# Optimization experiments

Hardware: AMD Instinct MI355X
Metric: run time of the kernel (lower is better)

The kernel has to match this reference:

```python
import jax, jax.numpy as jnp
import numpy as np

B, H, W, C = 1, 64, 64, 256
HEADS, K, DIL = 8, 7, 2
HD = C // HEADS
FF = 4 * C
EPS = 1e-5
SCALE = 1.0 / float(np.sqrt(HD))


def _axis_indices(L, k, d):
    """NATTEN dilated neighborhood: per dilation-group clamped sliding window.
    Returns key indices [L,k] and relative-position-bias indices [L,k]."""
    i = np.arange(L)
    g, rem = i // d, i % d                      # position within dilation group
    lg = (L - rem + d - 1) // d                 # group length per position
    start = np.clip(g - k // 2, 0, lg - k)      # clamped window start (group coords)
    a = np.arange(k)
    kidx = (start[:, None] + a[None, :]) * d + rem[:, None]          # key coord
    bidx = start[:, None] + a[None, :] - g[:, None] + (k - 1)        # rpb coord in [0, 2k-2]
    return kidx.astype(np.int32), bidx.astype(np.int32)


def setup_inputs():
    key = jax.random.key(0)
    ks = jax.random.split(key, 8)
    p = lambda k_, sh: jax.random.normal(k_, sh, jnp.float32) * 0.02
    return {
        "x": jax.random.normal(ks[0], (B, H, W, C), jnp.float32),
        "ln1_g": jnp.ones((C,), jnp.float32), "ln1_b": jnp.zeros((C,), jnp.float32),
        "wq": p(ks[1], (C, C)), "bq": jnp.zeros((C,), jnp.float32),
        "wk": p(ks[2], (C, C)), "bk": jnp.zeros((C,), jnp.float32),
        "wv": p(ks[3], (C, C)), "bv": jnp.zeros((C,), jnp.float32),
        "rpb": p(ks[4], (HEADS, 2 * K - 1, 2 * K - 1)),
        "wo": p(ks[5], (C, C)), "bo": jnp.zeros((C,), jnp.float32),
        "ln2_g": jnp.ones((C,), jnp.float32), "ln2_b": jnp.zeros((C,), jnp.float32),
        "w1": p(ks[6], (C, FF)), "b1": jnp.zeros((FF,), jnp.float32),
        "w2": p(ks[7], (FF, C)), "b2": jnp.zeros((C,), jnp.float32),
    }


def _layer_norm(x, g, b):
    m = jnp.mean(x, -1, keepdims=True)
    v = jnp.mean(jnp.square(x - m), -1, keepdims=True)
    return (x - m) * jax.lax.rsqrt(v + EPS) * g + b


def reference(x, ln1_g, ln1_b, wq, bq, wk, bk, wv, bv, rpb, wo, bo,
              ln2_g, ln2_b, w1, b1, w2, b2):
    ih, bih = _axis_indices(H, K, DIL)   # [H,K]
    iw, biw = _axis_indices(W, K, DIL)   # [W,K]
    hs = _layer_norm(x, ln1_g, ln1_b)
    q = (hs @ wq + bq).reshape(B, H, W, HEADS, HD) * SCALE
    k = (hs @ wk + bk).reshape(B, H, W, HEADS, HD)
    v = (hs @ wv + bv).reshape(B, H, W, HEADS, HD)
    # gather dilated neighborhoods -> [B,H,W,K,K,heads,hd]
    k_nb = k[:, ih[:, None, :, None], iw[None, :, None, :], :, :]
    v_nb = v[:, ih[:, None, :, None], iw[None, :, None, :], :, :]
    # natten2dqkrpb: per-query scores over K*K dilated neighbors + rpb
    scores = jnp.einsum('bijnc,bijklnc->bnijkl', q, k_nb)
    bias = rpb[:, bih[:, None, :, None], biw[None, :, None, :]]  # [heads,H,W,K,K]
    scores = scores + bias[None]
    probs = jax.nn.softmax(scores.reshape(B, HEADS, H, W, K * K), axis=-1)
    # natten2dav
    ctx = jnp.einsum('bnijp,bijpnc->bijnc', probs,
                     v_nb.reshape(B, H, W, K * K, HEADS, HD))
    attn_out = ctx.reshape(B, H, W, C) @ wo + bo
    hs2 = x + attn_out                      # residual (layer_scale disabled: init 0.0)
    y = _layer_norm(hs2, ln2_g, ln2_b)
    y = jax.nn.gelu(y @ w1 + b1, approximate=False) @ w2 + b2
    return hs2 + y
```

## Files before the change

### kernel.cpp

```cpp
#include <hip/hip_runtime.h>
#include <math.h>

#define CC 256
#define NTOK 4096
#define NHEADS 8
#define HD 32
#define FFD 1024
#define LN_EPS 1e-5f
#define QSCALE 0.17677669529663687f

typedef __bf16 bf16x8 __attribute__((ext_vector_type(8)));
typedef float f32x4 __attribute__((ext_vector_type(4)));
typedef unsigned short u16x8 __attribute__((ext_vector_type(8)));

__device__ __forceinline__ unsigned short f2bf(float f) {
    unsigned u = __builtin_bit_cast(unsigned, f);
    u += 0x7fff + ((u >> 16) & 1);
    return (unsigned short)(u >> 16);
}
__device__ __forceinline__ float bf2f(unsigned short h) {
    unsigned u = ((unsigned)h) << 16;
    return __builtin_bit_cast(float, u);
}
__device__ __forceinline__ void gload16(const unsigned short* g, unsigned short* l) {
    __builtin_amdgcn_global_load_lds(
        (const __attribute__((address_space(1))) unsigned int*)(const void*)g,
        (__attribute__((address_space(3))) unsigned int*)(void*)l, 16, 0, 0);
}

__global__ void ln_kernel(const float* __restrict__ x, const float* __restrict__ g,
                          const float* __restrict__ b, unsigned short* __restrict__ out) {
    int wave = threadIdx.x >> 6;
    int lane = threadIdx.x & 63;
    int tok = blockIdx.x * 4 + wave;
    const float4 v = ((const float4*)(x + (size_t)tok * CC))[lane];
    float s  = v.x + v.y + v.z + v.w;
    float ss = v.x * v.x + v.y * v.y + v.z * v.z + v.w * v.w;
    #pragma unroll
    for (int o = 32; o > 0; o >>= 1) { s += __shfl_xor(s, o); ss += __shfl_xor(ss, o); }
    float m   = s * (1.0f / CC);
    float var = ss * (1.0f / CC) - m * m;
    float r   = rsqrtf(var + LN_EPS);
    float4 gv = ((const float4*)g)[lane];
    float4 bv = ((const float4*)b)[lane];
    ushort4 o4;
    o4.x = f2bf((v.x - m) * r * gv.x + bv.x);
    o4.y = f2bf((v.y - m) * r * gv.y + bv.y);
    o4.z = f2bf((v.z - m) * r * gv.z + bv.z);
    o4.w = f2bf((v.w - m) * r * gv.w + bv.w);
    ((ushort4*)(out + (size_t)tok * CC))[lane] = o4;
}

__global__ void setup_kernel(const float* __restrict__ wq, const float* __restrict__ wk,
                             const float* __restrict__ wv, const float* __restrict__ wo,
                             const float* __restrict__ w1, const float* __restrict__ w2,
                             const float* __restrict__ bq, const float* __restrict__ bk,
                             const float* __restrict__ bv,
                             unsigned short* __restrict__ wt_qkv, unsigned short* __restrict__ wo_t,
                             unsigned short* __restrict__ w1_t, unsigned short* __restrict__ w2_t,
                             float* __restrict__ bqkv) {
    int id = blockIdx.x;
    int t = threadIdx.x;
    if (id == 192) {
        bqkv[t]       = bq[t] * QSCALE;
        bqkv[256 + t] = bk[t];
        bqkv[512 + t] = bv[t];
        return;
    }
    const float* src; unsigned short* dst;
    int Kd, N, rowoff = 0, bx, by; float scale = 1.0f;
    if (id < 16)       { src = wq; dst = wt_qkv; Kd = 256;  N = 256;  scale = QSCALE; int l = id;       bx = l & 3;  by = l >> 2; }
    else if (id < 32)  { src = wk; dst = wt_qkv; Kd = 256;  N = 256;  rowoff = 256;   int l = id - 16;  bx = l & 3;  by = l >> 2; }
    else if (id < 48)  { src = wv; dst = wt_qkv; Kd = 256;  N = 256;  rowoff = 512;   int l = id - 32;  bx = l & 3;  by = l >> 2; }
    else if (id < 64)  { src = wo; dst = wo_t;   Kd = 256;  N = 256;                  int l = id - 48;  bx = l & 3;  by = l >> 2; }
    else if (id < 128) { src = w1; dst = w1_t;   Kd = 256;  N = 1024;                 int l = id - 64;  bx = l & 15; by = l >> 4; }
    else               { src = w2; dst = w2_t;   Kd = 1024; N = 256;                  int l = id - 128; bx = l & 3;  by = l >> 2; }
    int n0 = bx * 64, k0 = by * 64;
    __shared__ float tile[64][65];
    int cc = t & 63, rb = t >> 6;
    #pragma unroll
    for (int i = 0; i < 16; i++) {
        int r = rb + i * 4;
        tile[r][cc] = src[(size_t)(k0 + r) * N + n0 + cc];
    }
    __syncthreads();
    int n = t >> 2;
    #pragma unroll
    for (int i = 0; i < 8; i++) {
        int p = (t & 3) + i * 4;
        unsigned lo = f2bf(tile[2 * p][n] * scale);
        unsigned hi = f2bf(tile[2 * p + 1][n] * scale);
        *(unsigned*)(dst + (size_t)(rowoff + n0 + n) * Kd + k0 + 2 * p) = lo | (hi << 16);
    }
}

template<int BM, int BN, int KD, int ACT, bool ADD_RES, bool OUT_BF16>
__global__ __launch_bounds__(256) void gemm_db(
    const unsigned short* __restrict__ A, const unsigned short* __restrict__ Bt,
    const float* __restrict__ bias, const float* __restrict__ res,
    void* __restrict__ Cm, int N) {
    constexpr int WM = BM / 2, WN = BN / 2;
    constexpr int MF = WM / 16, NF = WN / 16;
    constexpr int NIT = KD / 64;
    __shared__ unsigned short lds[2][(BM + BN) * 64];
    const int t = threadIdx.x;
    const int lane = t & 63, w = t >> 6;
    const int wr = w >> 1, wc = w & 1;
    const int bm = blockIdx.y * BM, bn = blockIdx.x * BN;
    const int fr = lane & 15, sq = lane >> 4;

    auto stage = [&](int it, int buf) {
        unsigned short* La = lds[buf];
        unsigned short* Lb = lds[buf] + BM * 64;
        #pragma unroll
        for (int i = 0; i < BM * 8 / 256; i++) {
            int c = t + i * 256;
            int kk = c / (BM * 4), r = (c % (BM * 4)) >> 2, jj = c & 3;
            gload16(A + (size_t)(bm + r) * KD + it * 64 + kk * 32 + jj * 8, La + c * 8);
        }
        #pragma unroll
        for (int i = 0; i < BN * 8 / 256; i++) {
            int c = t + i * 256;
            int kk = c / (BN * 4), r = (c % (BN * 4)) >> 2, jj = c & 3;
            gload16(Bt + (size_t)(bn + r) * KD + it * 64 + kk * 32 + jj * 8, Lb + c * 8);
        }
    };

    f32x4 acc[MF][NF] = {};
    stage(0, 0);
    for (int it = 0; it < NIT; ++it) {
        const int buf = it & 1;
        __syncthreads();
        if (it + 1 < NIT) stage(it + 1, buf ^ 1);
        #pragma unroll
        for (int kk = 0; kk < 2; kk++) {
            const char* La = (const char*)(lds[buf]) + kk * BM * 64;
            const char* Lb = (const char*)(lds[buf] + BM * 64) + kk * BN * 64;
            bf16x8 af[MF], bfr[NF];
            #pragma unroll
            for (int i = 0; i < MF; i++)
                af[i] = *(const bf16x8*)(La + (wr * WM + i * 16 + fr) * 64 + sq * 16);
            #pragma unroll
            for (int j = 0; j < NF; j++)
                bfr[j] = *(const bf16x8*)(Lb + (wc * WN + j * 16 + fr) * 64 + sq * 16);
            #pragma unroll
            for (int i = 0; i < MF; i++)
                #pragma unroll
                for (int j = 0; j < NF; j++)
                    acc[i][j] = __builtin_amdgcn_mfma_f32_16x16x32_bf16(af[i], bfr[j], acc[i][j], 0, 0, 0);
        }
    }
    #pragma unroll
    for (int i = 0; i < MF; i++) {
        int row0 = bm + wr * WM + i * 16 + sq * 4;
        #pragma unroll
        for (int j = 0; j < NF; j++) {
            int col = bn + wc * WN + j * 16 + fr;
            float bvv = bias[col];
            #pragma unroll
            for (int r = 0; r < 4; r++) {
                float v = acc[i][j][r] + bvv;
                if constexpr (ACT == 1) v = 0.5f * v * (1.0f + erff(v * 0.70710678118654752f));
                if constexpr (ADD_RES) v += res[(size_t)(row0 + r) * N + col];
                if constexpr (OUT_BF16)
                    ((unsigned short*)Cm)[(size_t)(row0 + r) * N + col] = f2bf(v);
                else
                    ((float*)Cm)[(size_t)(row0 + r) * N + col] = v;
            }
        }
    }
}

__global__ __launch_bounds__(256) void attn_mfma(
    const unsigned short* __restrict__ qkv, const float* __restrict__ rpb,
    unsigned short* __restrict__ ctx) {
    __shared__ __align__(16) unsigned short VT[128][136];
    __shared__ __align__(16) unsigned short Pl[4][16][136];
    __shared__ unsigned short tbl[16][112];
    __shared__ float rpbl[4][172];

    const int t = threadIdx.x;
    const int lane = t & 63, w = t >> 6;
    const int fr = lane & 15, sq = lane >> 4;
    const int bid = blockIdx.x;
    const int p = bid & 3, tile = (bid >> 2) & 63, hb = bid >> 8;
    const int ri = p >> 1, rj = p & 1;
    const int tgi = (tile >> 3) * 4, tgj = (tile & 7) * 4;
    const int kgi0 = min(max(tgi - 3, 0), 22);
    const int kgj0 = min(max(tgj - 3, 0), 22);
    const int head = hb * 4 + w;

    for (int i = lane; i < 169; i += 64)
        rpbl[w][i] = rpb[head * 169 + i];
    if (lane == 0) rpbl[w][169] = -1e30f;

    for (int e = t; e < 16 * 112; e += 256) {
        int q = e / 112, kk = e % 112;
        unsigned short idx = 169;
        if (kk < 100) {
            int kr = kk / 10, kc = kk % 10;
            int qgi = tgi + (q >> 2), qgj = tgj + (q & 3);
            int kgi = kgi0 + kr, kgj = kgj0 + kc;
            int si = min(max(qgi - 3, 0), 25), sj = min(max(qgj - 3, 0), 25);
            if (kgi >= si && kgi <= si + 6 && kgj >= sj && kgj <= sj + 6)
                idx = (unsigned short)((kgi - qgi + 6) * 13 + (kgj - qgj + 6));
        }
        tbl[q][kk] = idx;
    }

    for (int c0 = t; c0 < 1600; c0 += 256) {
        int key = c0 >> 4, ch8 = c0 & 15;
        int kr = key / 10, kc = key % 10;
        int kt = ((kgi0 + kr) * 2 + ri) * 64 + (kgj0 + kc) * 2 + rj;
        u16x8 vv = *(const u16x8*)(qkv + (size_t)kt * 768 + 512 + hb * 128 + ch8 * 8);
        #pragma unroll
        for (int e = 0; e < 8; e++) VT[ch8 * 8 + e][key] = vv[e];
    }
    for (int c0 = t; c0 < 128 * 14; c0 += 256) {
        int row = c0 / 14, cp = c0 % 14;
        *(unsigned*)&VT[row][100 + cp * 2] = 0;
    }
    __syncthreads();

    const int qtok = ((tgi + (fr >> 2)) * 2 + ri) * 64 + (tgj + (fr & 3)) * 2 + rj;
    bf16x8 qf = *(const bf16x8*)(qkv + (size_t)qtok * 768 + head * 32 + sq * 8);

    f32x4 sc[7];
    #pragma unroll
    for (int c = 0; c < 7; c++) {
        int kk = c * 16 + fr;
        if (kk > 99) kk = 99;
        int kr = kk / 10, kc = kk % 10;
        int kt = ((kgi0 + kr) * 2 + ri) * 64 + (kgj0 + kc) * 2 + rj;
        bf16x8 kf = *(const bf16x8*)(qkv + (size_t)kt * 768 + 256 + head * 32 + sq * 8);
        f32x4 z = {0.0f, 0.0f, 0.0f, 0.0f};
        sc[c] = __builtin_amdgcn_mfma_f32_16x16x32_bf16(kf, qf, z, 0, 0, 0);
    }
    #pragma unroll
    for (int c = 0; c < 7; c++)
        #pragma unroll
        for (int r = 0; r < 4; r++) {
            int idx = tbl[fr][c * 16 + 4 * sq + r];
            sc[c][r] += rpbl[w][idx];
        }

    float mx = -1e30f;
    #pragma unroll
    for (int c = 0; c < 7; c++)
        #pragma unroll
        for (int r = 0; r < 4; r++) mx = fmaxf(mx, sc[c][r]);
    mx = fmaxf(mx, __shfl_xor(mx, 16));
    mx = fmaxf(mx, __shfl_xor(mx, 32));
    float sum = 0.0f;
    #pragma unroll
    for (int c = 0; c < 7; c++)
        #pragma unroll
        for (int r = 0; r < 4; r++) {
            sc[c][r] = __expf(sc[c][r] - mx);
            sum += sc[c][r];
        }
    sum += __shfl_xor(sum, 16);
    sum += __shfl_xor(sum, 32);
    float inv = 1.0f / sum;

    #pragma unroll
    for (int c = 0; c < 7; c++)
        #pragma unroll
        for (int r = 0; r < 4; r++)
            Pl[w][fr][c * 16 + 4 * sq + r] = f2bf(sc[c][r] * inv);
    *(unsigned long long*)&Pl[w][fr][112 + sq * 4] = 0ull;

    f32x4 o0 = {0, 0, 0, 0}, o1 = {0, 0, 0, 0};
    #pragma unroll
    for (int m = 0; m < 4; m++) {
        bf16x8 pf = *(const bf16x8*)(&Pl[w][fr][m * 32 + sq * 8]);
        bf16x8 v0 = *(const bf16x8*)(&VT[w * 32 + fr][m * 32 + sq * 8]);
        bf16x8 v1 = *(const bf16x8*)(&VT[w * 32 + 16 + fr][m * 32 + sq * 8]);
        o0 = __builtin_amdgcn_mfma_f32_16x16x32_bf16(pf, v0, o0, 0, 0, 0);
        o1 = __builtin_amdgcn_mfma_f32_16x16x32_bf16(pf, v1, o1, 0, 0, 0);
    }
    #pragma unroll
    for (int r = 0; r < 4; r++) {
        int tok = ((tgi + sq) * 2 + ri) * 64 + (tgj + r) * 2 + rj;
        ctx[(size_t)tok * 256 + head * 32 + fr]      = f2bf(o0[r]);
        ctx[(size_t)tok * 256 + head * 32 + 16 + fr] = f2bf(o1[r]);
    }
}

extern "C" void kernel_launch(void* const* d_in, const int* in_sizes, int n_in,
                              void* d_out, int out_size, void* d_ws, size_t ws_size,
                              hipStream_t stream) {
    const float* x     = (const float*)d_in[0];
    const float* ln1_g = (const float*)d_in[1];
    const float* ln1_b = (const float*)d_in[2];
    const float* wq    = (const float*)d_in[3];
    const float* bq    = (const float*)d_in[4];
    const float* wk    = (const float*)d_in[5];
    const float* bk    = (const float*)d_in[6];
    const float* wv    = (const float*)d_in[7];
    const float* bv    = (const float*)d_in[8];
    const float* rpb   = (const float*)d_in[9];
    const float* wo    = (const float*)d_in[10];
    const float* bo    = (const float*)d_in[11];
    const float* ln2_g = (const float*)d_in[12];
    const float* ln2_b = (const float*)d_in[13];
    const float* w1    = (const float*)d_in[14];
    const float* b1    = (const float*)d_in[15];
    const float* w2    = (const float*)d_in[16];
    const float* b2    = (const float*)d_in[17];

    char* wsb = (char*)d_ws;
    unsigned short* hs_bf  = (unsigned short*)(wsb);
    unsigned short* qkv_bf = (unsigned short*)(wsb + (2u << 20));
    unsigned short* ctx_bf = (unsigned short*)(wsb + (8u << 20));
    float*          hs2    = (float*)(wsb + (10u << 20));
    unsigned short* y1_bf  = (unsigned short*)(wsb + (14u << 20));
    unsigned short* gm_bf  = (unsigned short*)(wsb + (16u << 20));
    unsigned short* wt_qkv = (unsigned short*)(wsb + (24u << 20));
    unsigned short* wo_t   = wt_qkv + 768 * 256;
    unsigned short* w1_t   = wo_t + 256 * 256;
    unsigned short* w2_t   = w1_t + 1024 * 256;
    float*          bqkv   = (float*)(w2_t + 256 * 1024);

    setup_kernel<<<193, 256, 0, stream>>>(wq, wk, wv, wo, w1, w2, bq, bk, bv,
                                          wt_qkv, wo_t, w1_t, w2_t, bqkv);
    ln_kernel<<<NTOK / 4, 256, 0, stream>>>(x, ln1_g, ln1_b, hs_bf);
    gemm_db<64, 64, 256, 0, false, true><<<dim3(12, 64), 256, 0, stream>>>(
        hs_bf, wt_qkv, bqkv, nullptr, qkv_bf, 768);
    attn_mfma<<<512, 256, 0, stream>>>(qkv_bf, rpb, ctx_bf);
    gemm_db<32, 64, 256, 0, true, false><<<dim3(4, 128), 256, 0, stream>>>(
        ctx_bf, wo_t, bo, x, hs2, 256);
    ln_kernel<<<NTOK / 4, 256, 0, stream>>>(hs2, ln2_g, ln2_b, y1_bf);
    gemm_db<64, 64, 256, 1, false, true><<<dim3(16, 64), 256, 0, stream>>>(
        y1_bf, w1_t, b1, nullptr, gm_bf, 1024);
    gemm_db<32, 64, 1024, 0, true, false><<<dim3(4, 128), 256, 0, stream>>>(
        gm_bf, w2_t, b2, hs2, (float*)d_out, 256);
}
```

Baseline: 136.6 us.

## Pre-swizzle weights into MFMA fragment layout and load B directly from global

The setup kernel now writes the transposed bf16 weights in a per-lane MFMA fragment order, so the GEMM loads B fragments straight from global memory into registers with one-step prefetch instead of staging them through LDS. GEMM tiles grow to 128x64 and 64x64 with configurable warp layouts, which halves the grid. The first LayerNorm is folded into the setup kernel launch as extra blocks to remove one launch. The trade-off is more global traffic per wave for B, since it is no longer shared through LDS, and higher register pressure.

```diff
diff --git a/kernel.cpp b/kernel.cpp
--- a/kernel.cpp
+++ b/kernel.cpp
@@ -28,11 +28,9 @@
         (__attribute__((address_space(3))) unsigned int*)(void*)l, 16, 0, 0);
 }
 
-__global__ void ln_kernel(const float* __restrict__ x, const float* __restrict__ g,
-                          const float* __restrict__ b, unsigned short* __restrict__ out) {
-    int wave = threadIdx.x >> 6;
-    int lane = threadIdx.x & 63;
-    int tok = blockIdx.x * 4 + wave;
+__device__ __forceinline__ void ln_row(const float* __restrict__ x, const float* __restrict__ g,
+                                       const float* __restrict__ b, unsigned short* __restrict__ out,
+                                       int tok, int lane) {
     const float4 v = ((const float4*)(x + (size_t)tok * CC))[lane];
     float s  = v.x + v.y + v.z + v.w;
     float ss = v.x * v.x + v.y * v.y + v.z * v.z + v.w * v.w;
@@ -51,16 +49,27 @@
     ((ushort4*)(out + (size_t)tok * CC))[lane] = o4;
 }
 
+__global__ void ln_kernel(const float* __restrict__ x, const float* __restrict__ g,
+                          const float* __restrict__ b, unsigned short* __restrict__ out) {
+    ln_row(x, g, b, out, blockIdx.x * 4 + (threadIdx.x >> 6), threadIdx.x & 63);
+}
+
 __global__ void setup_kernel(const float* __restrict__ wq, const float* __restrict__ wk,
                              const float* __restrict__ wv, const float* __restrict__ wo,
                              const float* __restrict__ w1, const float* __restrict__ w2,
                              const float* __restrict__ bq, const float* __restrict__ bk,
                              const float* __restrict__ bv,
+                             const float* __restrict__ x, const float* __restrict__ ln1_g,
+                             const float* __restrict__ ln1_b,
                              unsigned short* __restrict__ wt_qkv, unsigned short* __restrict__ wo_t,
                              unsigned short* __restrict__ w1_t, unsigned short* __restrict__ w2_t,
-                             float* __restrict__ bqkv) {
+                             float* __restrict__ bqkv, unsigned short* __restrict__ hs_bf) {
     int id = blockIdx.x;
     int t = threadIdx.x;
+    if (id >= 193) {
+        ln_row(x, ln1_g, ln1_b, hs_bf, (id - 193) * 4 + (t >> 6), t & 63);
+        return;
+    }
     if (id == 192) {
         bqkv[t]       = bq[t] * QSCALE;
         bqkv[256 + t] = bk[t];
@@ -68,13 +77,13 @@
         return;
     }
     const float* src; unsigned short* dst;
-    int Kd, N, rowoff = 0, bx, by; float scale = 1.0f;
-    if (id < 16)       { src = wq; dst = wt_qkv; Kd = 256;  N = 256;  scale = QSCALE; int l = id;       bx = l & 3;  by = l >> 2; }
-    else if (id < 32)  { src = wk; dst = wt_qkv; Kd = 256;  N = 256;  rowoff = 256;   int l = id - 16;  bx = l & 3;  by = l >> 2; }
-    else if (id < 48)  { src = wv; dst = wt_qkv; Kd = 256;  N = 256;  rowoff = 512;   int l = id - 32;  bx = l & 3;  by = l >> 2; }
-    else if (id < 64)  { src = wo; dst = wo_t;   Kd = 256;  N = 256;                  int l = id - 48;  bx = l & 3;  by = l >> 2; }
-    else if (id < 128) { src = w1; dst = w1_t;   Kd = 256;  N = 1024;                 int l = id - 64;  bx = l & 15; by = l >> 4; }
-    else               { src = w2; dst = w2_t;   Kd = 1024; N = 256;                  int l = id - 128; bx = l & 3;  by = l >> 2; }
+    int N, rowoff16 = 0, bx, by, KC = 8; float scale = 1.0f;
+    if (id < 16)       { src = wq; dst = wt_qkv; N = 256;                  int l = id;       bx = l & 3;  by = l >> 2; scale = QSCALE; }
+    else if (id < 32)  { src = wk; dst = wt_qkv; N = 256;  rowoff16 = 16;  int l = id - 16;  bx = l & 3;  by = l >> 2; }
+    else if (id < 48)  { src = wv; dst = wt_qkv; N = 256;  rowoff16 = 32;  int l = id - 32;  bx = l & 3;  by = l >> 2; }
+    else if (id < 64)  { src = wo; dst = wo_t;   N = 256;                  int l = id - 48;  bx = l & 3;  by = l >> 2; }
+    else if (id < 128) { src = w1; dst = w1_t;   N = 1024;                 int l = id - 64;  bx = l & 15; by = l >> 4; }
+    else               { src = w2; dst = w2_t;   N = 256;  KC = 32;        int l = id - 128; bx = l & 3;  by = l >> 2; }
     int n0 = bx * 64, k0 = by * 64;
     __shared__ float tile[64][65];
     int cc = t & 63, rb = t >> 6;
@@ -84,70 +93,77 @@
         tile[r][cc] = src[(size_t)(k0 + r) * N + n0 + cc];
     }
     __syncthreads();
-    int n = t >> 2;
-    #pragma unroll
-    for (int i = 0; i < 8; i++) {
-        int p = (t & 3) + i * 4;
-        unsigned lo = f2bf(tile[2 * p][n] * scale);
-        unsigned hi = f2bf(tile[2 * p + 1][n] * scale);
-        *(unsigned*)(dst + (size_t)(rowoff + n0 + n) * Kd + k0 + 2 * p) = lo | (hi << 16);
-    }
-}
-
-template<int BM, int BN, int KD, int ACT, bool ADD_RES, bool OUT_BF16>
-__global__ __launch_bounds__(256) void gemm_db(
-    const unsigned short* __restrict__ A, const unsigned short* __restrict__ Bt,
+    int lane = t & 63, fr = lane & 15, sq = lane >> 4, ncl = t >> 6;
+    #pragma unroll
+    for (int kcl = 0; kcl < 2; kcl++) {
+        unsigned short tmp[8];
+        #pragma unroll
+        for (int e = 0; e < 8; e++)
+            tmp[e] = f2bf(tile[kcl * 32 + sq * 8 + e][ncl * 16 + fr] * scale);
+        int nc = rowoff16 + (n0 >> 4) + ncl;
+        int kc = (k0 >> 5) + kcl;
+        *(u16x8*)(dst + ((size_t)(nc * KC + kc) * 64 + lane) * 8) = *(const u16x8*)tmp;
+    }
+}
+
+template<int BM, int BN, int WARPS_M, int KD, int ACT, bool ADD_RES, bool OUT_BF16>
+__global__ __launch_bounds__(256) void gemm_v3(
+    const unsigned short* __restrict__ A, const unsigned short* __restrict__ Bf,
     const float* __restrict__ bias, const float* __restrict__ res,
     void* __restrict__ Cm, int N) {
-    constexpr int WM = BM / 2, WN = BN / 2;
+    constexpr int WARPS_N = 4 / WARPS_M;
+    constexpr int WM = BM / WARPS_M, WN = BN / WARPS_N;
     constexpr int MF = WM / 16, NF = WN / 16;
     constexpr int NIT = KD / 64;
-    __shared__ unsigned short lds[2][(BM + BN) * 64];
+    constexpr int KC = KD / 32;
+    __shared__ unsigned short lds[2][BM * 64];
     const int t = threadIdx.x;
     const int lane = t & 63, w = t >> 6;
-    const int wr = w >> 1, wc = w & 1;
+    const int wr = w / WARPS_N, wc = w % WARPS_N;
     const int bm = blockIdx.y * BM, bn = blockIdx.x * BN;
     const int fr = lane & 15, sq = lane >> 4;
+    const int ncb = (bn >> 4) + wc * NF;
 
     auto stage = [&](int it, int buf) {
         unsigned short* La = lds[buf];
-        unsigned short* Lb = lds[buf] + BM * 64;
-        #pragma unroll
-        for (int i = 0; i < BM * 8 / 256; i++) {
+        #pragma unroll
+        for (int i = 0; i < BM / 32; i++) {
             int c = t + i * 256;
-            int kk = c / (BM * 4), r = (c % (BM * 4)) >> 2, jj = c & 3;
-            gload16(A + (size_t)(bm + r) * KD + it * 64 + kk * 32 + jj * 8, La + c * 8);
-        }
-        #pragma unroll
-        for (int i = 0; i < BN * 8 / 256; i++) {
-            int c = t + i * 256;
-            int kk = c / (BN * 4), r = (c % (BN * 4)) >> 2, jj = c & 3;
-            gload16(Bt + (size_t)(bn + r) * KD + it * 64 + kk * 32 + jj * 8, Lb + c * 8);
+            int s32 = c / (BM * 4), r = (c % (BM * 4)) >> 2, jj = c & 3;
+            gload16(A + (size_t)(bm + r) * KD + it * 64 + s32 * 32 + jj * 8, La + c * 8);
         }
     };
+    auto loadB = [&](bf16x8* bfrag, int s) {
+        #pragma unroll
+        for (int j = 0; j < NF; j++)
+            bfrag[j] = *(const bf16x8*)(Bf + ((size_t)((ncb + j) * KC + s) * 64 + lane) * 8);
+    };
 
     f32x4 acc[MF][NF] = {};
+    bf16x8 bnext[NF];
     stage(0, 0);
+    loadB(bnext, 0);
     for (int it = 0; it < NIT; ++it) {
         const int buf = it & 1;
         __syncthreads();
         if (it + 1 < NIT) stage(it + 1, buf ^ 1);
         #pragma unroll
         for (int kk = 0; kk < 2; kk++) {
+            bf16x8 bcur[NF];
+            #pragma unroll
+            for (int j = 0; j < NF; j++) bcur[j] = bnext[j];
+            int s = it * 2 + kk + 1;
+            if (s < 2 * NIT) loadB(bnext, s);
             const char* La = (const char*)(lds[buf]) + kk * BM * 64;
-            const char* Lb = (const char*)(lds[buf] + BM * 64) + kk * BN * 64;
-            bf16x8 af[MF], bfr[NF];
+            bf16x8 af[MF];
             #pragma unroll
             for (int i = 0; i < MF; i++)
                 af[i] = *(const bf16x8*)(La + (wr * WM + i * 16 + fr) * 64 + sq * 16);
             #pragma unroll
-            for (int j = 0; j < NF; j++)
-                bfr[j] = *(const bf16x8*)(Lb + (wc * WN + j * 16 + fr) * 64 + sq * 16);
-            #pragma unroll
             for (int i = 0; i < MF; i++)
                 #pragma unroll
                 for (int j = 0; j < NF; j++)
-                    acc[i][j] = __builtin_amdgcn_mfma_f32_16x16x32_bf16(af[i], bfr[j], acc[i][j], 0, 0, 0);
+                    acc[i][j] = __builtin_amdgcn_mfma_f32_16x16x32_bf16(af[i], bcur[j], acc[i][j], 0, 0, 0);
         }
     }
     #pragma unroll
@@ -322,17 +338,17 @@
     unsigned short* w2_t   = w1_t + 1024 * 256;
     float*          bqkv   = (float*)(w2_t + 256 * 1024);
 
-    setup_kernel<<<193, 256, 0, stream>>>(wq, wk, wv, wo, w1, w2, bq, bk, bv,
-                                          wt_qkv, wo_t, w1_t, w2_t, bqkv);
-    ln_kernel<<<NTOK / 4, 256, 0, stream>>>(x, ln1_g, ln1_b, hs_bf);
-    gemm_db<64, 64, 256, 0, false, true><<<dim3(12, 64), 256, 0, stream>>>(
+    setup_kernel<<<1217, 256, 0, stream>>>(wq, wk, wv, wo, w1, w2, bq, bk, bv,
+                                           x, ln1_g, ln1_b,
+                                           wt_qkv, wo_t, w1_t, w2_t, bqkv, hs_bf);
+    gemm_v3<128, 64, 4, 256, 0, false, true><<<dim3(12, 32), 256, 0, stream>>>(
         hs_bf, wt_qkv, bqkv, nullptr, qkv_bf, 768);
     attn_mfma<<<512, 256, 0, stream>>>(qkv_bf, rpb, ctx_bf);
-    gemm_db<32, 64, 256, 0, true, false><<<dim3(4, 128), 256, 0, stream>>>(
+    gemm_v3<64, 64, 2, 256, 0, true, false><<<dim3(4, 64), 256, 0, stream>>>(
         ctx_bf, wo_t, bo, x, hs2, 256);
     ln_kernel<<<NTOK / 4, 256, 0, stream>>>(hs2, ln2_g, ln2_b, y1_bf);
-    gemm_db<64, 64, 256, 1, false, true><<<dim3(16, 64), 256, 0, stream>>>(
+    gemm_v3<128, 64, 4, 256, 1, false, true><<<dim3(16, 32), 256, 0, stream>>>(
         y1_bf, w1_t, b1, nullptr, gm_bf, 1024);
-    gemm_db<32, 64, 1024, 0, true, false><<<dim3(4, 128), 256, 0, stream>>>(
+    gemm_v3<64, 64, 2, 1024, 0, true, false><<<dim3(4, 64), 256, 0, stream>>>(
         gm_bf, w2_t, b2, hs2, (float*)d_out, 256);
 }
```

After: 145.3 us. 1.06x slower.
